# Kernel tuning notes

Hardware: AMD Instinct MI355X
Metric: run time of the kernel (lower is better)

## Reference

```python
import jax, jax.numpy as jnp
import numpy as np

DIM = 384
DIM_HEAD = 384
HEADS = 4
SCALE = (DIM_HEAD / HEADS) ** -0.5  # per-head dim 96


def _chan_layernorm(x, g, eps=1e-5):
    # LayerNorm over channel dim (axis=1), biased variance, scale only
    mean = jnp.mean(x, axis=1, keepdims=True)
    var = jnp.var(x, axis=1, keepdims=True)
    return (x - mean) * jax.lax.rsqrt(var + eps) * g


def setup_inputs() -> dict:
    key = jax.random.key(0)
    k0, k1, k2 = jax.random.split(key, 3)
    x = jax.random.normal(k0, (16, DIM, 64, 64), dtype=jnp.float32)
    prenorm_g = jnp.ones((1, DIM, 1, 1), dtype=jnp.float32)
    Wqkv = jax.random.normal(k1, (3 * DIM_HEAD, DIM), dtype=jnp.float32) * 0.02
    Wout = jax.random.normal(k2, (DIM, DIM_HEAD), dtype=jnp.float32) * 0.02
    bout = jnp.zeros((DIM,), dtype=jnp.float32)
    outnorm_g = jnp.ones((1, DIM, 1, 1), dtype=jnp.float32)
    return {"x": x, "prenorm_g": prenorm_g, "Wqkv": Wqkv,
            "Wout": Wout, "bout": bout, "outnorm_g": outnorm_g}


def reference(x, prenorm_g, Wqkv, Wout, bout, outnorm_g):
    b, c, h, w = x.shape
    n = h * w
    ch = DIM_HEAD // HEADS  # per-head channels

    xn = _chan_layernorm(x, prenorm_g)              # prenorm; residual uses this
    qkv = jnp.einsum('oc,bchw->bohw', Wqkv, xn)     # 1x1 conv, no bias
    q, k, v = jnp.split(qkv, 3, axis=1)             # each [b, dim_head, h, w]

    def to_heads(t):
        return t.reshape(b, HEADS, ch, n)           # b h c (x y)
    q, k, v = to_heads(q), to_heads(k), to_heads(v)

    q = jax.nn.softmax(q, axis=2) * SCALE           # softmax over channel dim
    k = jax.nn.softmax(k, axis=3)                   # softmax over spatial dim

    context = jnp.einsum('bhdn,bhen->bhde', k, v)   # [b,h,ch,ch]
    out = jnp.einsum('bhde,bhdn->bhen', context, q) # [b,h,ch,n]
    out = out.reshape(b, DIM_HEAD, h, w)

    out = jnp.einsum('oc,bchw->bohw', Wout, out) + bout[None, :, None, None]
    out = _chan_layernorm(out, outnorm_g)
    return out + xn
```

## Files before the change

kernel.cpp:

```cpp
#include <hip/hip_runtime.h>
#include <cstdint>
#include <cstddef>


#define P_     65536
#define P96_   6291456
#define ROW_   384
#define NS_    8
#define CHK_   512
#define SCALE_ 0.10206207261596577f
#define EPS_   1e-5f

typedef unsigned short us16;
typedef __attribute__((ext_vector_type(8))) unsigned short ushort8;
typedef __attribute__((ext_vector_type(8))) short short8;
typedef __attribute__((ext_vector_type(4))) float f32x4;

static __device__ __forceinline__ float bfu2f(us16 u) {
  union { float f; unsigned int i; } x; x.i = ((unsigned int)u) << 16; return x.f;
}
static __device__ __forceinline__ us16 f2bfu(float f) {
  union { float f; unsigned int u; } x; x.f = f;
  unsigned int r = x.u + 0x7fffu + ((x.u >> 16) & 1u);
  return (us16)(r >> 16);
}

#define GLDS16(gp, lp) \
  __builtin_amdgcn_global_load_lds((const __attribute__((address_space(1))) void*)(gp), \
                                   (__attribute__((address_space(3))) void*)(lp), 16, 0, 0)

__global__ __launch_bounds__(256) void k_wcvt(const float* __restrict__ wqkv,
                                              const float* __restrict__ wout,
                                              us16* __restrict__ wbf) {
  int i = (blockIdx.x * 256 + threadIdx.x) * 4;
  const float* s = (i < 442368) ? (wqkv + i) : (wout + (i - 442368));
  wbf[i + 0] = f2bfu(s[0]); wbf[i + 1] = f2bfu(s[1]);
  wbf[i + 2] = f2bfu(s[2]); wbf[i + 3] = f2bfu(s[3]);
}

__global__ __launch_bounds__(256) void k_prenorm(const float* __restrict__ x,
                                                 const float* __restrict__ g,
                                                 us16* __restrict__ xn) {
  __shared__ float gs[384];
  __shared__ float sm[4][64], sq[4][64];
  int t = threadIdx.x;
  for (int c = t; c < 384; c += 256) gs[c] = g[c];
  int qd = t >> 6, pb = t & 63;
  int p = blockIdx.x * 64 + pb;
  int b = p >> 12, pix = p & 4095;
  const float* xb = x + (size_t)b * 1572864 + pix;
  float xv[96];
  float s1 = 0.f, s2 = 0.f;
  #pragma unroll
  for (int i = 0; i < 96; ++i) {
    float v = xb[(size_t)(qd * 96 + i) * 4096];
    xv[i] = v; s1 += v; s2 += v * v;
  }
  sm[qd][pb] = s1; sq[qd][pb] = s2;
  __syncthreads();
  float su = sm[0][pb] + sm[1][pb] + sm[2][pb] + sm[3][pb];
  float ss = sq[0][pb] + sq[1][pb] + sq[2][pb] + sq[3][pb];
  float mean = su * (1.f / 384);
  float var = ss * (1.f / 384) - mean * mean;
  float rs = rsqrtf(var + EPS_);
  us16* ob = xn + (size_t)p * ROW_ + qd * 96;
  #pragma unroll
  for (int c8 = 0; c8 < 12; ++c8) {
    ushort8 u;
    #pragma unroll
    for (int j = 0; j < 8; ++j)
      u[j] = f2bfu((xv[c8 * 8 + j] - mean) * rs * gs[qd * 96 + c8 * 8 + j]);
    *(ushort8*)(ob + c8 * 8) = u;
  }
}

__global__ __launch_bounds__(256) void k_gemm(const us16* __restrict__ src,
                                              const us16* __restrict__ W,
                                              us16* __restrict__ dst,
                                              int MT, int mode) {
  __shared__ __align__(16) us16 As[128 * 32];
  __shared__ __align__(16) us16 Bs[128 * 32];
  int i = blockIdx.x;
  int xcd = i & 7, idx = i >> 3;
  int ot = idx % MT;
  int pt = (idx / MT) * 8 + xcd;
  int p0 = pt * 128, o0 = ot * 128;
  int tid = threadIdx.x;
  int wv = tid >> 6, l = tid & 63;
  int wr = wv >> 1, wc = wv & 1;
  int lm = l & 15, kq = l >> 4;

  f32x4 acc[4][4];
  #pragma unroll
  for (int a = 0; a < 4; ++a)
    #pragma unroll
    for (int q = 0; q < 4; ++q) acc[a][q] = (f32x4)0.f;

  int lrow = l >> 2, lcol = (l & 3) * 8;

  for (int k0 = 0; k0 < 384; k0 += 32) {
    #pragma unroll
    for (int c = 0; c < 2; ++c) {
      int ra = wv * 32 + c * 16;
      GLDS16(src + (size_t)(p0 + ra + lrow) * ROW_ + k0 + lcol, &As[ra * 32]);
      GLDS16(W   + (size_t)(o0 + ra + lrow) * ROW_ + k0 + lcol, &Bs[ra * 32]);
    }
    __syncthreads();
    const short8* A8 = (const short8*)As;
    const short8* B8 = (const short8*)Bs;
    short8 af[4], bf[4];
    #pragma unroll
    for (int ii = 0; ii < 4; ++ii) af[ii] = A8[(wr * 64 + ii * 16 + lm) * 4 + kq];
    #pragma unroll
    for (int jj = 0; jj < 4; ++jj) bf[jj] = B8[(wc * 64 + jj * 16 + lm) * 4 + kq];
    #pragma unroll
    for (int ii = 0; ii < 4; ++ii)
      #pragma unroll
      for (int jj = 0; jj < 4; ++jj)
        acc[ii][jj] = __builtin_amdgcn_mfma_f32_16x16x32_bf16(af[ii], bf[jj], acc[ii][jj], 0, 0, 0);
    __syncthreads();
  }

  #pragma unroll
  for (int ii = 0; ii < 4; ++ii) {
    int prow = p0 + wr * 64 + ii * 16 + kq * 4;
    #pragma unroll
    for (int jj = 0; jj < 4; ++jj) {
      int o = o0 + wc * 64 + jj * 16 + lm;
      f32x4 v = acc[ii][jj];
      if (mode) {
        #pragma unroll
        for (int r = 0; r < 4; ++r)
          dst[(size_t)(prow + r) * ROW_ + o] = f2bfu(v[r]);
      } else {
        int sec = o / 96, d = o % 96;
        if (sec < 4) {
          #pragma unroll
          for (int r = 0; r < 4; ++r)
            dst[(size_t)sec * P96_ + (size_t)(prow + r) * 96 + d] = f2bfu(v[r]);
        } else {
          bool isk = sec < 8;
          alignas(8) us16 buf[4];
          #pragma unroll
          for (int r = 0; r < 4; ++r) {
            float f = v[r];
            if (isk) f = __expf(f);
            buf[r] = f2bfu(f);
          }
          *(uint2*)(dst + (size_t)sec * P96_ + (size_t)d * P_ + prow) = *(const uint2*)buf;
        }
      }
    }
  }
}

__global__ __launch_bounds__(256) void k_ctx(const us16* __restrict__ qkv,
                                             float* __restrict__ ctxs,
                                             float* __restrict__ zs) {
  __shared__ __align__(16) us16 Ek[96 * 64];
  __shared__ __align__(16) us16 Vv[96 * 64];
  int bh = blockIdx.x, s = blockIdx.y;
  int b = bh >> 2, h = bh & 3;
  const us16* kb = qkv + (size_t)(4 + h) * P96_;
  const us16* vb = qkv + (size_t)(8 + h) * P96_;
  int pbase = b * 4096 + s * CHK_;
  int t = threadIdx.x;
  int wv = t >> 6, l = t & 63;
  int wr = wv >> 1, wc = wv & 1;
  int lm = l & 15, kq = l >> 4;

  f32x4 acc[3][3];
  f32x4 accz[3];
  #pragma unroll
  for (int a = 0; a < 3; ++a) {
    accz[a] = (f32x4)0.f;
    #pragma unroll
    for (int q = 0; q < 3; ++q) acc[a][q] = (f32x4)0.f;
  }
  short8 vone;
  #pragma unroll
  for (int j = 0; j < 8; ++j) vone[j] = (short)0x3F80;

  int srow = wv * 24 + (l >> 3);
  int sgrp = l & 7;

  for (int tile = 0; tile < CHK_ / 64; ++tile) {
    int p0 = pbase + tile * 64;
    #pragma unroll
    for (int c = 0; c < 3; ++c) {
      int r = srow + c * 8;
      int g = sgrp ^ (r & 7);
      GLDS16(kb + (size_t)r * P_ + p0 + g * 8, &Ek[(wv * 24 + c * 8) * 64]);
      GLDS16(vb + (size_t)r * P_ + p0 + g * 8, &Vv[(wv * 24 + c * 8) * 64]);
    }
    __syncthreads();
    const short8* A8 = (const short8*)Ek;
    const short8* B8 = (const short8*)Vv;
    #pragma unroll
    for (int ks = 0; ks < 2; ++ks) {
      short8 af[3], bf[3];
      #pragma unroll
      for (int ii = 0; ii < 3; ++ii) {
        int m = wr * 48 + ii * 16 + lm;
        af[ii] = A8[m * 8 + (((ks * 4 + kq) ^ m) & 7) + ((ks * 4 + kq) & 8)];
        int e = wc * 48 + ii * 16 + lm;
        bf[ii] = B8[e * 8 + (((ks * 4 + kq) ^ e) & 7) + ((ks * 4 + kq) & 8)];
      }
      #pragma unroll
      for (int ii = 0; ii < 3; ++ii)
        #pragma unroll
        for (int jj = 0; jj < 3; ++jj)
          acc[ii][jj] = __builtin_amdgcn_mfma_f32_16x16x32_bf16(af[ii], bf[jj], acc[ii][jj], 0, 0, 0);
      if (wc == 0) {
        #pragma unroll
        for (int ii = 0; ii < 3; ++ii)
          accz[ii] = __builtin_amdgcn_mfma_f32_16x16x32_bf16(af[ii], vone, accz[ii], 0, 0, 0);
      }
    }
    __syncthreads();
  }

  float* cb = ctxs + (size_t)(s * 64 + bh) * 9216;
  #pragma unroll
  for (int ii = 0; ii < 3; ++ii) {
    int m0 = wr * 48 + ii * 16 + kq * 4;
    #pragma unroll
    for (int jj = 0; jj < 3; ++jj) {
      int e = wc * 48 + jj * 16 + lm;
      #pragma unroll
      for (int r = 0; r < 4; ++r)
        cb[(size_t)(m0 + r) * 96 + e] = acc[ii][jj][r];
    }
  }
  if (wc == 0 && lm == 0) {
    #pragma unroll
    for (int ii = 0; ii < 3; ++ii) {
      int m0 = wr * 48 + ii * 16 + kq * 4;
      #pragma unroll
      for (int r = 0; r < 4; ++r)
        zs[(size_t)(s * 64 + bh) * 96 + m0 + r] = accz[ii][r];
    }
  }
}

__global__ __launch_bounds__(256) void k_ctxred(const float* __restrict__ ctxs,
                                                const float* __restrict__ zs,
                                                float* __restrict__ ctx,
                                                float* __restrict__ zr) {
  int bh = blockIdx.x / 9, part = blockIdx.x % 9;
  int t = threadIdx.x;
  int idx = part * 1024 + t * 4;
  f32x4 sum = (f32x4)0.f;
  #pragma unroll
  for (int s = 0; s < NS_; ++s)
    sum += *(const f32x4*)&ctxs[(size_t)(s * 64 + bh) * 9216 + idx];
  *(f32x4*)&ctx[(size_t)bh * 9216 + idx] = sum;
  if (part == 0 && t < 96) {
    float z = 0.f;
    #pragma unroll
    for (int s = 0; s < NS_; ++s) z += zs[(size_t)(s * 64 + bh) * 96 + t];
    zr[bh * 96 + t] = z;
  }
}

__global__ __launch_bounds__(256) void k_attout(const us16* __restrict__ qkv,
                                                const float* __restrict__ ctx,
                                                const float* __restrict__ zr,
                                                us16* __restrict__ attout) {
  __shared__ float cs[9216];
  __shared__ float zrs[96];
  int bh = blockIdx.y, b = bh >> 2, h = bh & 3;
  int t = threadIdx.x;
  const float* cb = ctx + (size_t)bh * 9216;
  for (int i = t; i < 9216; i += 256) cs[i] = cb[i];
  if (t < 96) zrs[t] = 1.0f / zr[bh * 96 + t];
  __syncthreads();
  int p = b * 4096 + blockIdx.x * 256 + t;
  const us16* qrow = qkv + (size_t)h * P96_ + (size_t)p * 96;
  float qv[96];
  #pragma unroll
  for (int c8 = 0; c8 < 12; ++c8) {
    ushort8 u = *(const ushort8*)(qrow + c8 * 8);
    #pragma unroll
    for (int j = 0; j < 8; ++j) qv[c8 * 8 + j] = bfu2f(u[j]);
  }
  float m = -1e30f;
  #pragma unroll
  for (int d = 0; d < 96; ++d) m = fmaxf(m, qv[d]);
  float s = 0.f;
  #pragma unroll
  for (int d = 0; d < 96; ++d) { qv[d] = __expf(qv[d] - m); s += qv[d]; }
  float sc = SCALE_ / s;
  #pragma unroll
  for (int d = 0; d < 96; ++d) qv[d] *= sc * zrs[d];
  us16* ob = attout + (size_t)p * ROW_ + h * 96;
  #pragma unroll 1
  for (int e0 = 0; e0 < 96; e0 += 8) {
    float a0 = 0, a1 = 0, a2 = 0, a3 = 0, a4 = 0, a5 = 0, a6 = 0, a7 = 0;
    #pragma unroll
    for (int d = 0; d < 96; ++d) {
      float qd = qv[d];
      f32x4 c0 = *(const f32x4*)&cs[d * 96 + e0];
      f32x4 c1 = *(const f32x4*)&cs[d * 96 + e0 + 4];
      a0 += qd * c0[0]; a1 += qd * c0[1]; a2 += qd * c0[2]; a3 += qd * c0[3];
      a4 += qd * c1[0]; a5 += qd * c1[1]; a6 += qd * c1[2]; a7 += qd * c1[3];
    }
    ushort8 u;
    u[0] = f2bfu(a0); u[1] = f2bfu(a1); u[2] = f2bfu(a2); u[3] = f2bfu(a3);
    u[4] = f2bfu(a4); u[5] = f2bfu(a5); u[6] = f2bfu(a6); u[7] = f2bfu(a7);
    *(ushort8*)(ob + e0) = u;
  }
}

__global__ __launch_bounds__(256) void k_outnorm(const us16* __restrict__ y,
                                                 const us16* __restrict__ xn,
                                                 const float* __restrict__ bout,
                                                 const float* __restrict__ g,
                                                 float* __restrict__ out) {
  __shared__ float bs[384], gs[384];
  int t = threadIdx.x;
  for (int c = t; c < 384; c += 256) { bs[c] = bout[c]; gs[c] = g[c]; }
  __syncthreads();
  int p = blockIdx.x * 256 + t;
  int b = p >> 12, pix = p & 4095;
  const us16* yb = y + (size_t)p * ROW_;
  const us16* xb = xn + (size_t)p * ROW_;
  float sum = 0.f, sq = 0.f;
  #pragma unroll 4
  for (int c8 = 0; c8 < 48; ++c8) {
    ushort8 u = *(const ushort8*)(yb + c8 * 8);
    #pragma unroll
    for (int j = 0; j < 8; ++j) {
      float v = bfu2f(u[j]) + bs[c8 * 8 + j];
      sum += v; sq += v * v;
    }
  }
  float mean = sum * (1.f / 384);
  float var = sq * (1.f / 384) - mean * mean;
  float rs = rsqrtf(var + EPS_);
  float* oB = out + (size_t)b * 1572864 + pix;
  #pragma unroll 2
  for (int c8 = 0; c8 < 48; ++c8) {
    ushort8 u = *(const ushort8*)(yb + c8 * 8);
    ushort8 ux = *(const ushort8*)(xb + c8 * 8);
    #pragma unroll
    for (int j = 0; j < 8; ++j) {
      int c = c8 * 8 + j;
      float v = bfu2f(u[j]) + bs[c];
      oB[(size_t)c * 4096] = (v - mean) * rs * gs[c] + bfu2f(ux[j]);
    }
  }
}

extern "C" void kernel_launch(void* const* d_in, const int* in_sizes, int n_in,
                              void* d_out, int out_size, void* d_ws, size_t ws_size,
                              hipStream_t stream) {
  const float* x    = (const float*)d_in[0];
  const float* pg   = (const float*)d_in[1];
  const float* wqkv = (const float*)d_in[2];
  const float* wout = (const float*)d_in[3];
  const float* bout = (const float*)d_in[4];
  const float* og   = (const float*)d_in[5];

  char* ws = (char*)d_ws;
  us16*  xn     = (us16*)(ws);
  us16*  qkv    = (us16*)(ws + 50331648);
  us16*  attout = (us16*)(ws + 201326592);
  float* ctxred = (float*)(ws + 251658240);
  float* zred   = (float*)(ws + 254017536);
  us16*  wbf    = (us16*)(ws + 254042112);
  us16*  y      = qkv;
  float* out    = (float*)d_out;
  float* ctxs = (float*)d_out;
  float* zs   = (float*)((char*)d_out + 18874368);

  k_wcvt<<<576, 256, 0, stream>>>(wqkv, wout, wbf);
  k_prenorm<<<1024, 256, 0, stream>>>(x, pg, xn);
  k_gemm<<<4608, 256, 0, stream>>>(xn, wbf, qkv, 9, 0);
  k_ctx<<<dim3(64, NS_), 256, 0, stream>>>(qkv, ctxs, zs);
  k_ctxred<<<576, 256, 0, stream>>>(ctxs, zs, ctxred, zred);
  k_attout<<<dim3(16, 64), 256, 0, stream>>>(qkv, ctxred, zred, attout);
  k_gemm<<<1536, 256, 0, stream>>>(attout, wbf + 442368, y, 3, 1);
  k_outnorm<<<256, 256, 0, stream>>>(y, xn, bout, og, out);
}
```

Measured before the change: 498.2 us.

## Pipeline GEMM with triple-buffered LDS, 64-wide K tiles and 256x128 blocks

Rewrites the bf16 MFMA GEMM so each 512-thread block computes a 256x128 output tile. K is walked in six 64-wide steps through a three-stage LDS ring with XOR-swizzled addresses and explicit vmcnt waits, so global-to-LDS loads for the next two stages overlap with MFMA work. Wave priority is raised during the MFMA section. This aims to hide load latency and cut barrier stalls and LDS bank conflicts, at the cost of 144 KB of LDS per block and tighter occupancy.

```diff
diff --git a/kernel.cpp b/kernel.cpp
--- a/kernel.cpp
+++ b/kernel.cpp
@@ -74,21 +74,47 @@
   }
 }
 
-__global__ __launch_bounds__(256) void k_gemm(const us16* __restrict__ src,
-                                              const us16* __restrict__ W,
-                                              us16* __restrict__ dst,
-                                              int MT, int mode) {
-  __shared__ __align__(16) us16 As[128 * 32];
-  __shared__ __align__(16) us16 Bs[128 * 32];
+__global__ __launch_bounds__(512, 2) void k_gemm(const us16* __restrict__ src,
+                                                 const us16* __restrict__ W,
+                                                 us16* __restrict__ dst,
+                                                 int MT, int mode) {
+  __shared__ __align__(16) us16 As[3 * 16384];
+  __shared__ __align__(16) us16 Bs[3 * 8192];
   int i = blockIdx.x;
   int xcd = i & 7, idx = i >> 3;
   int ot = idx % MT;
   int pt = (idx / MT) * 8 + xcd;
-  int p0 = pt * 128, o0 = ot * 128;
+  int p0 = pt * 256, o0 = ot * 128;
   int tid = threadIdx.x;
   int wv = tid >> 6, l = tid & 63;
   int wr = wv >> 1, wc = wv & 1;
   int lm = l & 15, kq = l >> 4;
+  int lr = l >> 3, lg = l & 7;
+
+  const us16* aB[4]; const us16* bB[2];
+  int swz = (lg ^ lr) * 8;
+  #pragma unroll
+  for (int r = 0; r < 4; ++r)
+    aB[r] = src + (size_t)(p0 + 64 * r + 8 * wv + lr) * ROW_ + swz;
+  #pragma unroll
+  for (int r = 0; r < 2; ++r)
+    bB[r] = W + (size_t)(o0 + 64 * r + 8 * wv + lr) * ROW_ + swz;
+
+  int aidx[4][2], bidx[4][2];
+  #pragma unroll
+  for (int ii = 0; ii < 4; ++ii) {
+    int row = wr * 64 + ii * 16 + lm;
+    #pragma unroll
+    for (int ks = 0; ks < 2; ++ks)
+      aidx[ii][ks] = row * 8 + ((ks * 4 + kq) ^ (row & 7));
+  }
+  #pragma unroll
+  for (int jj = 0; jj < 4; ++jj) {
+    int row = wc * 64 + jj * 16 + lm;
+    #pragma unroll
+    for (int ks = 0; ks < 2; ++ks)
+      bidx[jj][ks] = row * 8 + ((ks * 4 + kq) ^ (row & 7));
+  }
 
   f32x4 acc[4][4];
   #pragma unroll
@@ -96,30 +122,47 @@
     #pragma unroll
     for (int q = 0; q < 4; ++q) acc[a][q] = (f32x4)0.f;
 
-  int lrow = l >> 2, lcol = (l & 3) * 8;
-
-  for (int k0 = 0; k0 < 384; k0 += 32) {
-    #pragma unroll
-    for (int c = 0; c < 2; ++c) {
-      int ra = wv * 32 + c * 16;
-      GLDS16(src + (size_t)(p0 + ra + lrow) * ROW_ + k0 + lcol, &As[ra * 32]);
-      GLDS16(W   + (size_t)(o0 + ra + lrow) * ROW_ + k0 + lcol, &Bs[ra * 32]);
-    }
-    __syncthreads();
-    const short8* A8 = (const short8*)As;
-    const short8* B8 = (const short8*)Bs;
-    short8 af[4], bf[4];
-    #pragma unroll
-    for (int ii = 0; ii < 4; ++ii) af[ii] = A8[(wr * 64 + ii * 16 + lm) * 4 + kq];
-    #pragma unroll
-    for (int jj = 0; jj < 4; ++jj) bf[jj] = B8[(wc * 64 + jj * 16 + lm) * 4 + kq];
-    #pragma unroll
-    for (int ii = 0; ii < 4; ++ii)
-      #pragma unroll
-      for (int jj = 0; jj < 4; ++jj)
-        acc[ii][jj] = __builtin_amdgcn_mfma_f32_16x16x32_bf16(af[ii], bf[jj], acc[ii][jj], 0, 0, 0);
-    __syncthreads();
-  }
+#define STG(t_, b_) do { \
+    _Pragma("unroll") \
+    for (int r_ = 0; r_ < 4; ++r_) \
+      GLDS16(aB[r_] + (t_) * 64, &As[(b_) * 16384 + (64 * r_ + 8 * wv) * 64]); \
+    _Pragma("unroll") \
+    for (int r_ = 0; r_ < 2; ++r_) \
+      GLDS16(bB[r_] + (t_) * 64, &Bs[(b_) * 8192 + (64 * r_ + 8 * wv) * 64]); \
+  } while (0)
+
+  STG(0, 0);
+  STG(1, 1);
+  asm volatile("s_waitcnt vmcnt(6)\n\ts_barrier" ::: "memory");
+
+  #pragma unroll
+  for (int t = 0; t < 6; ++t) {
+    if (t + 2 < 6) STG(t + 2, (t + 2) % 3);
+    const short8* A8 = (const short8*)As + (t % 3) * 2048;
+    const short8* B8 = (const short8*)Bs + (t % 3) * 1024;
+    __builtin_amdgcn_s_setprio(1);
+    #pragma unroll
+    for (int ks = 0; ks < 2; ++ks) {
+      short8 af[4], bf[4];
+      #pragma unroll
+      for (int ii = 0; ii < 4; ++ii) af[ii] = A8[aidx[ii][ks]];
+      #pragma unroll
+      for (int jj = 0; jj < 4; ++jj) bf[jj] = B8[bidx[jj][ks]];
+      #pragma unroll
+      for (int ii = 0; ii < 4; ++ii)
+        #pragma unroll
+        for (int jj = 0; jj < 4; ++jj)
+          acc[ii][jj] = __builtin_amdgcn_mfma_f32_16x16x32_bf16(af[ii], bf[jj], acc[ii][jj], 0, 0, 0);
+    }
+    __builtin_amdgcn_s_setprio(0);
+    if (t < 5) {
+      if (t + 2 < 6)
+        asm volatile("s_waitcnt vmcnt(6) lgkmcnt(0)\n\ts_barrier" ::: "memory");
+      else
+        asm volatile("s_waitcnt vmcnt(0) lgkmcnt(0)\n\ts_barrier" ::: "memory");
+    }
+  }
+#undef STG
 
   #pragma unroll
   for (int ii = 0; ii < 4; ++ii) {
@@ -376,10 +419,10 @@
 
   k_wcvt<<<576, 256, 0, stream>>>(wqkv, wout, wbf);
   k_prenorm<<<1024, 256, 0, stream>>>(x, pg, xn);
-  k_gemm<<<4608, 256, 0, stream>>>(xn, wbf, qkv, 9, 0);
+  k_gemm<<<2304, 512, 0, stream>>>(xn, wbf, qkv, 9, 0);
   k_ctx<<<dim3(64, NS_), 256, 0, stream>>>(qkv, ctxs, zs);
   k_ctxred<<<576, 256, 0, stream>>>(ctxs, zs, ctxred, zred);
   k_attout<<<dim3(16, 64), 256, 0, stream>>>(qkv, ctxred, zred, attout);
-  k_gemm<<<1536, 256, 0, stream>>>(attout, wbf + 442368, y, 3, 1);
+  k_gemm<<<768, 512, 0, stream>>>(attout, wbf + 442368, y, 3, 1);
   k_outnorm<<<256, 256, 0, stream>>>(y, xn, bout, og, out);
 }
```

Result: no change. 502.9 us (+0.9%).
